# Optimization experiments

Hardware: AMD Instinct MI355X
Metric: run time of the kernel (lower is better)

The kernel has to match this reference:

```python
import jax, jax.numpy as jnp
import numpy as np

N, E, IN, HID, OUT = 100000, 1600000, 128, 128, 64


def setup_inputs() -> dict:
    key = jax.random.key(0)
    k1, k2, k3, k4 = jax.random.split(key, 4)
    x = jax.random.normal(k1, (N, IN), dtype=jnp.float32)
    edge_index = jax.random.randint(k2, (2, E), 0, N, dtype=jnp.int64)
    W1 = jax.random.normal(k3, (IN, HID), dtype=jnp.float32) * (1.0 / np.sqrt(IN))
    b1 = jnp.zeros((HID,), dtype=jnp.float32)
    W2 = jax.random.normal(k4, (HID, OUT), dtype=jnp.float32) * (1.0 / np.sqrt(HID))
    b2 = jnp.zeros((OUT,), dtype=jnp.float32)
    return {"x": x, "edge_index": edge_index, "W1": W1, "b1": b1, "W2": W2, "b2": b2}


def _gcn_conv(x, src, dst, norm, W, b):
    # linear transform first (PyG order when reducing feature dim), then SpMM
    h = x @ W                                   # [N, F_out]
    msg = h[src] * norm[:, None]                # [E+N, F_out] gathered messages
    out = jax.ops.segment_sum(msg, dst, num_segments=x.shape[0])
    return out + b


def _norm_coeffs(edge_index, num_nodes, dtype):
    # add self-loops and compute symmetric normalization deg^-1/2[src]*deg^-1/2[dst]
    loop = jnp.arange(num_nodes, dtype=edge_index.dtype)
    src = jnp.concatenate([edge_index[0], loop])
    dst = jnp.concatenate([edge_index[1], loop])
    deg = jax.ops.segment_sum(jnp.ones_like(dst, dtype=dtype), dst, num_segments=num_nodes)
    dinv = jnp.where(deg > 0, jax.lax.rsqrt(jnp.maximum(deg, 1.0)), 0.0)
    norm = dinv[src] * dinv[dst]
    return src, dst, norm


def reference(x, edge_index, W1, b1, W2, b2):
    # eval-mode forward: dropout is identity
    src, dst, norm = _norm_coeffs(edge_index, x.shape[0], x.dtype)
    h = jax.nn.relu(_gcn_conv(x, src, dst, norm, W1, b1))
    out = _gcn_conv(h, src, dst, norm, W2, b2)
    return out
```

## Files before the change

kernel.cpp:

```cpp
#include <hip/hip_runtime.h>
#include <hip/hip_bf16.h>

#define DEVINL __device__ __forceinline__

typedef __attribute__((ext_vector_type(8))) short bf16x8;
typedef __attribute__((ext_vector_type(4))) float f32x4;

union U8 {
    bf16x8 v;
    uint4 u;
};

DEVINL int clampidx(int v, int n) { return ((unsigned)v < (unsigned)n) ? v : 0; }
DEVINL float bflo(unsigned int u) { return __uint_as_float(u << 16); }
DEVINL float bfhi(unsigned int u) { return __uint_as_float(u & 0xffff0000u); }
DEVINL unsigned int f2bf(float f) {
    unsigned int u = __float_as_uint(f);
    u += 0x7fffu + ((u >> 16) & 1u);
    return u >> 16;
}

DEVINL void split8(const float4 v0, const float4 v1, uint4& hi, uint4& lo) {
    const float xv[8] = {v0.x, v0.y, v0.z, v0.w, v1.x, v1.y, v1.z, v1.w};
    unsigned h[8], l[8];
#pragma unroll
    for (int j = 0; j < 8; ++j) {
        h[j] = f2bf(xv[j]);
        const float r = xv[j] - bflo(h[j]);
        l[j] = f2bf(r);
    }
    hi = make_uint4(h[0] | (h[1] << 16), h[2] | (h[3] << 16),
                    h[4] | (h[5] << 16), h[6] | (h[7] << 16));
    lo = make_uint4(l[0] | (l[1] << 16), l[2] | (l[3] << 16),
                    l[4] | (l[5] << 16), l[6] | (l[7] << 16));
}

__global__ __launch_bounds__(256) void k_count_wprep(
    const int* __restrict__ ei, int* __restrict__ bktCnt, int E, int n,
    const float* __restrict__ W1, const float* __restrict__ W2,
    unsigned short* __restrict__ WT1h, unsigned short* __restrict__ WT1l,
    unsigned short* __restrict__ WT2h, unsigned short* __restrict__ WT2l) {
    __shared__ int hist[1024];
    const int gi = blockIdx.x * 256 + threadIdx.x;
    if (gi < 16384) {
        const int nn = gi & 127, k = gi >> 7;
        const float v = W1[k * 128 + nn];
        const unsigned h = f2bf(v);
        const float r = v - bflo(h);
        WT1h[nn * 128 + k] = (unsigned short)h;
        WT1l[nn * 128 + k] = (unsigned short)f2bf(r);
    }
    if (gi < 8192) {
        const int nn = gi & 63, k = gi >> 6;
        const float v = W2[k * 64 + nn];
        const unsigned h = f2bf(v);
        const float r = v - bflo(h);
        WT2h[nn * 128 + k] = (unsigned short)h;
        WT2l[nn * 128 + k] = (unsigned short)f2bf(r);
    }
    for (int i = threadIdx.x; i < 1024; i += 256) hist[i] = 0;
    __syncthreads();
    const int base = blockIdx.x * 4096;
#pragma unroll
    for (int j = 0; j < 16; ++j) {
        int i = base + j * 256 + threadIdx.x;
        if (i < E) atomicAdd(&hist[clampidx(ei[(size_t)E + i], n) >> 7], 1);
    }
    __syncthreads();
    for (int b = threadIdx.x; b < 1024; b += 256) {
        int c = hist[b];
        if (c) atomicAdd(&bktCnt[b], c);
    }
}

__global__ __launch_bounds__(256) void k_bktscan(const int* __restrict__ bktCnt,
                                                 int* __restrict__ bktBase,
                                                 int* __restrict__ bktCur, int NB) {
    __shared__ int sh[256];
    int carry = 0;
    for (int c0 = 0; c0 < NB; c0 += 256) {
        const int i = c0 + threadIdx.x;
        const int v = (i < NB) ? bktCnt[i] : 0;
        sh[threadIdx.x] = v;
        __syncthreads();
        for (int off = 1; off < 256; off <<= 1) {
            int t = (threadIdx.x >= off) ? sh[threadIdx.x - off] : 0;
            __syncthreads();
            sh[threadIdx.x] += t;
            __syncthreads();
        }
        if (i < NB) {
            const int excl = carry + sh[threadIdx.x] - v;
            bktBase[i] = excl;
            bktCur[i] = excl;
        }
        const int tot = sh[255];
        __syncthreads();
        carry += tot;
    }
    if (threadIdx.x == 0) bktBase[NB] = carry;
}

__global__ __launch_bounds__(256) void k_bktscatter(const int* __restrict__ ei,
                                                    int* __restrict__ bktCur,
                                                    unsigned int* __restrict__ packed,
                                                    int E, int n) {
    __shared__ unsigned int sPack[4096];
    __shared__ unsigned short sBkt[4096];
    __shared__ int sHist[1024], sStart[1024], sLoc[1024];
    for (int i = threadIdx.x; i < 1024; i += 256) {
        sHist[i] = 0;
        sLoc[i] = 0;
    }
    __syncthreads();
    const int base = blockIdx.x * 4096;
#pragma unroll
    for (int j = 0; j < 16; ++j) {
        const int k = j * 256 + threadIdx.x;
        const int i = base + k;
        if (i < E) {
            const int s = clampidx(ei[i], n);
            const int d = clampidx(ei[(size_t)E + i], n);
            const int b = d >> 7;
            sPack[k] = ((unsigned)(d & 127) << 25) | (unsigned)s;
            sBkt[k] = (unsigned short)b;
            atomicAdd(&sHist[b], 1);
        }
    }
    __syncthreads();
    for (int b = threadIdx.x; b < 1024; b += 256) {
        const int c = sHist[b];
        sStart[b] = c ? atomicAdd(&bktCur[b], c) : 0;
    }
    __syncthreads();
#pragma unroll
    for (int j = 0; j < 16; ++j) {
        const int k = j * 256 + threadIdx.x;
        const int i = base + k;
        if (i < E) {
            const int b = sBkt[k];
            const int pos = sStart[b] + atomicAdd(&sLoc[b], 1);
            packed[pos] = sPack[k];
        }
    }
}

__global__ __launch_bounds__(256) void k_bktfill(const unsigned int* __restrict__ packed,
                                                 const int* __restrict__ bktBase,
                                                 int* __restrict__ p, float* __restrict__ dinv,
                                                 int* __restrict__ srcs, int n) {
    constexpr int CAP = 8192;
    __shared__ unsigned int sPack[CAP];
    __shared__ int sSrc[CAP];
    __shared__ int deg[128], incl[128], cur[128];
    const int bkt = blockIdx.x;
    const int e0 = bktBase[bkt], e1 = bktBase[bkt + 1];
    const int cnt = e1 - e0;
    const int tid = threadIdx.x;
    if (tid < 128) deg[tid] = 0;
    __syncthreads();
    for (int i = tid; i < cnt; i += 256) {
        const unsigned int u = packed[e0 + i];
        if (i < CAP) sPack[i] = u;
        atomicAdd(&deg[u >> 25], 1);
    }
    __syncthreads();
    if (tid < 128) incl[tid] = deg[tid];
    __syncthreads();
    for (int off = 1; off < 128; off <<= 1) {
        const int v = (tid < 128 && tid >= off) ? incl[tid - off] : 0;
        __syncthreads();
        if (tid < 128) incl[tid] += v;
        __syncthreads();
    }
    const int node0 = bkt << 7;
    if (tid < 128) {
        cur[tid] = incl[tid] - deg[tid];
        const int node = node0 + tid;
        if (node < n) {
            p[node] = e0 + incl[tid];
            dinv[node] = rsqrtf((float)deg[tid] + 1.0f);
        }
    }
    __syncthreads();
    for (int i = tid; i < cnt; i += 256) {
        const unsigned int u = (i < CAP) ? sPack[i] : packed[e0 + i];
        const int dl = (int)(u >> 25);
        const int s = (int)(u & 0x1FFFFFFu);
        const int pos = atomicAdd(&cur[dl], 1);
        if (pos < CAP) sSrc[pos] = s;
        else srcs[e0 + pos] = s;
    }
    __syncthreads();
    const int lim = cnt < CAP ? cnt : CAP;
    for (int i = tid; i < lim; i += 256) srcs[e0 + i] = sSrc[i];
}

__global__ __launch_bounds__(256) void k_gemm1(const float* __restrict__ x,
                                               const unsigned short* __restrict__ WTh,
                                               const unsigned short* __restrict__ WTl,
                                               unsigned short* __restrict__ Y16, int n) {
    const int lane = threadIdx.x & 63;
    const int row16 = lane & 15;
    const int kg = lane >> 4;
    const int rowbase = blockIdx.x * 128 + (threadIdx.x >> 6) * 32;

    U8 ahi[2][4], alo[2][4];
#pragma unroll
    for (int g = 0; g < 2; ++g) {
        const int grow = rowbase + g * 16 + row16;
        if (grow < n) {
            const float* xp = x + (size_t)grow * 128 + kg * 8;
#pragma unroll
            for (int k0 = 0; k0 < 4; ++k0) {
                const float4 v0 = *(const float4*)(xp + k0 * 32);
                const float4 v1 = *(const float4*)(xp + k0 * 32 + 4);
                split8(v0, v1, ahi[g][k0].u, alo[g][k0].u);
            }
        } else {
#pragma unroll
            for (int k0 = 0; k0 < 4; ++k0) {
                ahi[g][k0].u = make_uint4(0, 0, 0, 0);
                alo[g][k0].u = make_uint4(0, 0, 0, 0);
            }
        }
    }

    f32x4 acc[2][8];
#pragma unroll
    for (int g = 0; g < 2; ++g)
#pragma unroll
        for (int nt = 0; nt < 8; ++nt) acc[g][nt] = (f32x4){0.f, 0.f, 0.f, 0.f};

#pragma unroll
    for (int nt = 0; nt < 8; ++nt) {
        const unsigned short* bp = WTh + (size_t)(nt * 16 + row16) * 128 + kg * 8;
        const unsigned short* bq = WTl + (size_t)(nt * 16 + row16) * 128 + kg * 8;
#pragma unroll
        for (int k0 = 0; k0 < 4; ++k0) {
            U8 bh, bl;
            bh.u = *(const uint4*)(bp + k0 * 32);
            bl.u = *(const uint4*)(bq + k0 * 32);
            acc[0][nt] = __builtin_amdgcn_mfma_f32_16x16x32_bf16(ahi[0][k0].v, bh.v, acc[0][nt], 0, 0, 0);
            acc[0][nt] = __builtin_amdgcn_mfma_f32_16x16x32_bf16(alo[0][k0].v, bh.v, acc[0][nt], 0, 0, 0);
            acc[0][nt] = __builtin_amdgcn_mfma_f32_16x16x32_bf16(ahi[0][k0].v, bl.v, acc[0][nt], 0, 0, 0);
            acc[1][nt] = __builtin_amdgcn_mfma_f32_16x16x32_bf16(ahi[1][k0].v, bh.v, acc[1][nt], 0, 0, 0);
            acc[1][nt] = __builtin_amdgcn_mfma_f32_16x16x32_bf16(alo[1][k0].v, bh.v, acc[1][nt], 0, 0, 0);
            acc[1][nt] = __builtin_amdgcn_mfma_f32_16x16x32_bf16(ahi[1][k0].v, bl.v, acc[1][nt], 0, 0, 0);
        }
    }

    const int m4 = (lane >> 4) * 4;
#pragma unroll
    for (int g = 0; g < 2; ++g)
#pragma unroll
        for (int nt = 0; nt < 8; ++nt) {
#pragma unroll
            for (int r = 0; r < 4; ++r) {
                const int orow = rowbase + g * 16 + m4 + r;
                if (orow < n)
                    Y16[(size_t)orow * 128 + nt * 16 + row16] =
                        (unsigned short)f2bf(acc[g][nt][r]);
            }
        }
}

__global__ __launch_bounds__(256) void k_gemm2_mfma(const unsigned short* __restrict__ H16,
                                                    const unsigned short* __restrict__ WTh,
                                                    const unsigned short* __restrict__ WTl,
                                                    unsigned short* __restrict__ Y16, int n) {
    const int lane = threadIdx.x & 63;
    const int row16 = lane & 15;
    const int kg = lane >> 4;
    const int rowbase = blockIdx.x * 64 + (threadIdx.x >> 6) * 16;
    const int grow = rowbase + row16;

    U8 a[4];
    if (grow < n) {
        const unsigned short* ap = H16 + (size_t)grow * 128 + kg * 8;
#pragma unroll
        for (int k0 = 0; k0 < 4; ++k0) a[k0].u = *(const uint4*)(ap + k0 * 32);
    } else {
#pragma unroll
        for (int k0 = 0; k0 < 4; ++k0) a[k0].u = make_uint4(0, 0, 0, 0);
    }

    f32x4 acc[4];
#pragma unroll
    for (int nt = 0; nt < 4; ++nt) acc[nt] = (f32x4){0.f, 0.f, 0.f, 0.f};

#pragma unroll
    for (int nt = 0; nt < 4; ++nt) {
        const unsigned short* bp = WTh + (size_t)(nt * 16 + row16) * 128 + kg * 8;
        const unsigned short* bq = WTl + (size_t)(nt * 16 + row16) * 128 + kg * 8;
#pragma unroll
        for (int k0 = 0; k0 < 4; ++k0) {
            U8 bh, bl;
            bh.u = *(const uint4*)(bp + k0 * 32);
            bl.u = *(const uint4*)(bq + k0 * 32);
            acc[nt] = __builtin_amdgcn_mfma_f32_16x16x32_bf16(a[k0].v, bh.v, acc[nt], 0, 0, 0);
            acc[nt] = __builtin_amdgcn_mfma_f32_16x16x32_bf16(a[k0].v, bl.v, acc[nt], 0, 0, 0);
        }
    }

    const int m4 = (lane >> 4) * 4;
#pragma unroll
    for (int nt = 0; nt < 4; ++nt) {
#pragma unroll
        for (int r = 0; r < 4; ++r) {
            const int orow = rowbase + m4 + r;
            if (orow < n)
                Y16[(size_t)orow * 64 + nt * 16 + row16] = (unsigned short)f2bf(acc[nt][r]);
        }
    }
}

__global__ __launch_bounds__(256) void k_gather128(const unsigned int* __restrict__ XW,
                                                   const int* __restrict__ p,
                                                   const int* __restrict__ srcs,
                                                   const float* __restrict__ dinv,
                                                   const float* __restrict__ b1,
                                                   unsigned int* __restrict__ H1b, int n) {
    const int node = __builtin_amdgcn_readfirstlane(blockIdx.x * 4 + (threadIdx.x >> 6));
    if (node >= n) return;
    const int t = threadIdx.x & 63;
    const int start = (node == 0) ? 0 : p[node - 1];
    const int end = p[node];
    const float din = dinv[node];
    const unsigned int us = XW[(size_t)node * 64 + t];
    float a0 = bflo(us) * din, a1 = bfhi(us) * din;

    int c = start;
    for (; c + 16 <= end; c += 16) {
        int s[16];
#pragma unroll
        for (int k = 0; k < 16; ++k) s[k] = __builtin_amdgcn_readfirstlane(srcs[c + k]);
        float w[16];
        unsigned int u[16];
#pragma unroll
        for (int k = 0; k < 16; ++k) {
            w[k] = dinv[s[k]];
            u[k] = XW[((unsigned)s[k] << 6) + t];
        }
#pragma unroll
        for (int k = 0; k < 16; ++k) {
            a0 = fmaf(bflo(u[k]), w[k], a0);
            a1 = fmaf(bfhi(u[k]), w[k], a1);
        }
    }
    for (; c + 4 <= end; c += 4) {
        int s[4];
#pragma unroll
        for (int k = 0; k < 4; ++k) s[k] = __builtin_amdgcn_readfirstlane(srcs[c + k]);
        float w[4];
        unsigned int u[4];
#pragma unroll
        for (int k = 0; k < 4; ++k) {
            w[k] = dinv[s[k]];
            u[k] = XW[((unsigned)s[k] << 6) + t];
        }
#pragma unroll
        for (int k = 0; k < 4; ++k) {
            a0 = fmaf(bflo(u[k]), w[k], a0);
            a1 = fmaf(bfhi(u[k]), w[k], a1);
        }
    }
    for (; c < end; ++c) {
        const int s = __builtin_amdgcn_readfirstlane(srcs[c]);
        const float w = dinv[s];
        const unsigned int u = XW[((unsigned)s << 6) + t];
        a0 = fmaf(bflo(u), w, a0);
        a1 = fmaf(bfhi(u), w, a1);
    }
    const float r0 = fmaxf(fmaf(a0, din, b1[2 * t]), 0.0f);
    const float r1 = fmaxf(fmaf(a1, din, b1[2 * t + 1]), 0.0f);
    H1b[(size_t)node * 64 + t] = f2bf(r0) | (f2bf(r1) << 16);
}

__global__ __launch_bounds__(256) void k_gather64(const unsigned short* __restrict__ h2,
                                                  const int* __restrict__ p,
                                                  const int* __restrict__ srcs,
                                                  const float* __restrict__ dinv,
                                                  const float* __restrict__ b2,
                                                  float* __restrict__ out, int n) {
    const int node = __builtin_amdgcn_readfirstlane(blockIdx.x * 4 + (threadIdx.x >> 6));
    if (node >= n) return;
    const int t = threadIdx.x & 63;
    const int start = (node == 0) ? 0 : p[node - 1];
    const int end = p[node];
    const float din = dinv[node];
    float acc = bflo(h2[(size_t)node * 64 + t]) * din;

    int c = start;
    for (; c + 16 <= end; c += 16) {
        int s[16];
#pragma unroll
        for (int k = 0; k < 16; ++k) s[k] = __builtin_amdgcn_readfirstlane(srcs[c + k]);
        float w[16], v[16];
#pragma unroll
        for (int k = 0; k < 16; ++k) {
            w[k] = dinv[s[k]];
            v[k] = bflo(h2[((unsigned)s[k] << 6) + t]);
        }
#pragma unroll
        for (int k = 0; k < 16; ++k) acc = fmaf(v[k], w[k], acc);
    }
    for (; c + 4 <= end; c += 4) {
        int s[4];
#pragma unroll
        for (int k = 0; k < 4; ++k) s[k] = __builtin_amdgcn_readfirstlane(srcs[c + k]);
        float w[4], v[4];
#pragma unroll
        for (int k = 0; k < 4; ++k) {
            w[k] = dinv[s[k]];
            v[k] = bflo(h2[((unsigned)s[k] << 6) + t]);
        }
#pragma unroll
        for (int k = 0; k < 4; ++k) acc = fmaf(v[k], w[k], acc);
    }
    for (; c < end; ++c) {
        const int s = __builtin_amdgcn_readfirstlane(srcs[c]);
        const float w = dinv[s];
        acc = fmaf(bflo(h2[((unsigned)s << 6) + t]), w, acc);
    }
    out[(size_t)node * 64 + t] = fmaf(acc, din, b2[t]);
}

extern "C" void kernel_launch(void* const* d_in, const int* in_sizes, int n_in,
                              void* d_out, int out_size, void* d_ws, size_t ws_size,
                              hipStream_t stream) {
    const float* x  = (const float*)d_in[0];
    const int* ei   = (const int*)d_in[1];
    const float* W1 = (const float*)d_in[2];
    const float* b1 = (const float*)d_in[3];
    const float* W2 = (const float*)d_in[4];
    const float* b2 = (const float*)d_in[5];

    const int n = in_sizes[0] / 128;
    const int E = in_sizes[1] / 2;
    const int NB = (n + 127) >> 7;

    auto al = [](size_t b) { return (b + 255) & ~(size_t)255; };
    const size_t off_p    = 0;
    const size_t off_dinv = off_p + al((size_t)n * 4);
    const size_t off_srcs = off_dinv + al((size_t)n * 4);
    const size_t off_XW   = off_srcs + al((size_t)E * 4);
    const size_t off_H1b  = off_XW + al((size_t)n * 64 * 4);
    const size_t off_w1h  = off_H1b + al((size_t)n * 64 * 4);
    const size_t off_w1l  = off_w1h + al(128 * 128 * 2);
    const size_t off_w2h  = off_w1l + al(128 * 128 * 2);
    const size_t off_w2l  = off_w2h + al(64 * 128 * 2);
    const size_t need     = off_w2l + (size_t)64 * 128 * 2;
    const size_t off_pk   = off_H1b;
    const size_t off_bc   = off_pk + al((size_t)E * 4);
    const size_t off_bb   = off_bc + al(1024 * 4);
    const size_t off_bu   = off_bb + al(1025 * 4);
    const size_t csr_end  = off_bu + (size_t)1024 * 4;

    if (ws_size < need || NB > 1024 || csr_end > off_w1h) {
        hipMemsetAsync(d_out, 0, (size_t)out_size * 4, stream);
        return;
    }

    int*            p    = (int*)((char*)d_ws + off_p);
    float*          dinv = (float*)((char*)d_ws + off_dinv);
    int*            srcs = (int*)((char*)d_ws + off_srcs);
    unsigned int*   XW   = (unsigned int*)((char*)d_ws + off_XW);
    unsigned int*   H1b  = (unsigned int*)((char*)d_ws + off_H1b);
    unsigned int*   pk   = (unsigned int*)((char*)d_ws + off_pk);
    int*            bCnt = (int*)((char*)d_ws + off_bc);
    int*            bBase= (int*)((char*)d_ws + off_bb);
    int*            bCur = (int*)((char*)d_ws + off_bu);
    unsigned short* WT1h = (unsigned short*)((char*)d_ws + off_w1h);
    unsigned short* WT1l = (unsigned short*)((char*)d_ws + off_w1l);
    unsigned short* WT2h = (unsigned short*)((char*)d_ws + off_w2h);
    unsigned short* WT2l = (unsigned short*)((char*)d_ws + off_w2l);
    float*          out  = (float*)d_out;

    const int gEdge = (E + 4095) / 4096;
    const int gM1   = (n + 127) / 128;
    const int gM2   = (n + 63) / 64;
    const int gG    = (n + 3) / 4;

    hipMemsetAsync(bCnt, 0, 1024 * 4, stream);

    k_count_wprep<<<gEdge, 256, 0, stream>>>(ei, bCnt, E, n, W1, W2, WT1h, WT1l, WT2h, WT2l);

    k_gemm1<<<gM1, 256, 0, stream>>>(x, WT1h, WT1l, (unsigned short*)XW, n);

    k_bktscan<<<1, 256, 0, stream>>>(bCnt, bBase, bCur, NB);
    k_bktscatter<<<gEdge, 256, 0, stream>>>(ei, bCur, pk, E, n);
    k_bktfill<<<NB, 256, 0, stream>>>(pk, bBase, p, dinv, srcs, n);

    k_gather128<<<gG, 256, 0, stream>>>(XW, p, srcs, dinv, b1, H1b, n);

    k_gemm2_mfma<<<gM2, 256, 0, stream>>>((const unsigned short*)H1b, WT2h, WT2l,
                                          (unsigned short*)XW, n);

    k_gather64<<<gG, 256, 0, stream>>>((const unsigned short*)XW, p, srcs, dinv, b2, out, n);
}
```

Before: 343.9 us.

## Replace atomic bucket reservation with per-block histogram prefix scan

The count kernel now writes a per-block bucket histogram instead of atomically adding into global counters. A new column-wise scan kernel computes each block's deterministic offset within every bucket plus the bucket totals. The scatter kernel then starts from precomputed offsets, dropping its local histogram pass and its global atomics. This removes the memset and the contention on bucket counters, at the cost of an extra kernel launch and a strided read/write of a gEdge×1024 offset table.

Result: no change. 346.9 us (+0.9%).

```diff
diff --git a/kernel.cpp b/kernel.cpp
--- a/kernel.cpp
+++ b/kernel.cpp
@@ -36,7 +36,7 @@
 }
 
 __global__ __launch_bounds__(256) void k_count_wprep(
-    const int* __restrict__ ei, int* __restrict__ bktCnt, int E, int n,
+    const int* __restrict__ ei, int* __restrict__ blkHist, int E, int n,
     const float* __restrict__ W1, const float* __restrict__ W2,
     unsigned short* __restrict__ WT1h, unsigned short* __restrict__ WT1l,
     unsigned short* __restrict__ WT2h, unsigned short* __restrict__ WT2l) {
@@ -67,20 +67,43 @@
         if (i < E) atomicAdd(&hist[clampidx(ei[(size_t)E + i], n) >> 7], 1);
     }
     __syncthreads();
-    for (int b = threadIdx.x; b < 1024; b += 256) {
-        int c = hist[b];
-        if (c) atomicAdd(&bktCnt[b], c);
-    }
-}
-
-__global__ __launch_bounds__(256) void k_bktscan(const int* __restrict__ bktCnt,
-                                                 int* __restrict__ bktBase,
-                                                 int* __restrict__ bktCur, int NB) {
+    int* row = blkHist + (size_t)blockIdx.x * 1024;
+    for (int b = threadIdx.x; b < 1024; b += 256) row[b] = hist[b];
+}
+
+__global__ __launch_bounds__(256) void k_blkscan(const int* __restrict__ blkHist,
+                                                 int* __restrict__ blkOff,
+                                                 int* __restrict__ bktTot, int nBlk) {
+    __shared__ int sh[1024];
+    const int b = blockIdx.x;
+    const int tid = threadIdx.x;
+    for (int i = tid; i < 1024; i += 256)
+        sh[i] = (i < nBlk) ? blkHist[(size_t)i * 1024 + b] : 0;
+    __syncthreads();
+    for (int off = 1; off < 1024; off <<= 1) {
+        int t[4];
+#pragma unroll
+        for (int j = 0; j < 4; ++j) {
+            const int i = tid + j * 256;
+            t[j] = (i >= off) ? sh[i - off] : 0;
+        }
+        __syncthreads();
+#pragma unroll
+        for (int j = 0; j < 4; ++j) sh[tid + j * 256] += t[j];
+        __syncthreads();
+    }
+    for (int i = tid; i < nBlk; i += 256)
+        blkOff[(size_t)i * 1024 + b] = (i == 0) ? 0 : sh[i - 1];
+    if (tid == 0) bktTot[b] = sh[nBlk - 1];
+}
+
+__global__ __launch_bounds__(256) void k_bktscan(const int* __restrict__ bktTot,
+                                                 int* __restrict__ bktBase, int NB) {
     __shared__ int sh[256];
     int carry = 0;
     for (int c0 = 0; c0 < NB; c0 += 256) {
         const int i = c0 + threadIdx.x;
-        const int v = (i < NB) ? bktCnt[i] : 0;
+        const int v = (i < NB) ? bktTot[i] : 0;
         sh[threadIdx.x] = v;
         __syncthreads();
         for (int off = 1; off < 256; off <<= 1) {
@@ -89,11 +112,7 @@
             sh[threadIdx.x] += t;
             __syncthreads();
         }
-        if (i < NB) {
-            const int excl = carry + sh[threadIdx.x] - v;
-            bktBase[i] = excl;
-            bktCur[i] = excl;
-        }
+        if (i < NB) bktBase[i] = carry + sh[threadIdx.x] - v;
         const int tot = sh[255];
         __syncthreads();
         carry += tot;
@@ -102,15 +121,17 @@
 }
 
 __global__ __launch_bounds__(256) void k_bktscatter(const int* __restrict__ ei,
-                                                    int* __restrict__ bktCur,
+                                                    const int* __restrict__ bktBase,
+                                                    const int* __restrict__ blkOff,
                                                     unsigned int* __restrict__ packed,
                                                     int E, int n) {
     __shared__ unsigned int sPack[4096];
     __shared__ unsigned short sBkt[4096];
-    __shared__ int sHist[1024], sStart[1024], sLoc[1024];
-    for (int i = threadIdx.x; i < 1024; i += 256) {
-        sHist[i] = 0;
-        sLoc[i] = 0;
+    __shared__ int sStart[1024], sLoc[1024];
+    const int* offrow = blkOff + (size_t)blockIdx.x * 1024;
+    for (int b = threadIdx.x; b < 1024; b += 256) {
+        sStart[b] = bktBase[b] + offrow[b];
+        sLoc[b] = 0;
     }
     __syncthreads();
     const int base = blockIdx.x * 4096;
@@ -124,13 +145,7 @@
             const int b = d >> 7;
             sPack[k] = ((unsigned)(d & 127) << 25) | (unsigned)s;
             sBkt[k] = (unsigned short)b;
-            atomicAdd(&sHist[b], 1);
-        }
-    }
-    __syncthreads();
-    for (int b = threadIdx.x; b < 1024; b += 256) {
-        const int c = sHist[b];
-        sStart[b] = c ? atomicAdd(&bktCur[b], c) : 0;
+        }
     }
     __syncthreads();
 #pragma unroll
@@ -439,6 +454,7 @@
     const int n = in_sizes[0] / 128;
     const int E = in_sizes[1] / 2;
     const int NB = (n + 127) >> 7;
+    const int gEdge = (E + 4095) / 4096;
 
     auto al = [](size_t b) { return (b + 255) & ~(size_t)255; };
     const size_t off_p    = 0;
@@ -452,12 +468,13 @@
     const size_t off_w2l  = off_w2h + al(64 * 128 * 2);
     const size_t need     = off_w2l + (size_t)64 * 128 * 2;
     const size_t off_pk   = off_H1b;
-    const size_t off_bc   = off_pk + al((size_t)E * 4);
-    const size_t off_bb   = off_bc + al(1024 * 4);
-    const size_t off_bu   = off_bb + al(1025 * 4);
-    const size_t csr_end  = off_bu + (size_t)1024 * 4;
-
-    if (ws_size < need || NB > 1024 || csr_end > off_w1h) {
+    const size_t off_bh   = off_pk + al((size_t)E * 4);
+    const size_t off_bo   = off_bh + al((size_t)gEdge * 1024 * 4);
+    const size_t off_bt   = off_bo + al((size_t)gEdge * 1024 * 4);
+    const size_t off_bb   = off_bt + al(1024 * 4);
+    const size_t csr_end  = off_bb + (size_t)1025 * 4;
+
+    if (ws_size < need || NB > 1024 || gEdge > 1024 || csr_end > off_w1h) {
         hipMemsetAsync(d_out, 0, (size_t)out_size * 4, stream);
         return;
     }
@@ -468,28 +485,28 @@
     unsigned int*   XW   = (unsigned int*)((char*)d_ws + off_XW);
     unsigned int*   H1b  = (unsigned int*)((char*)d_ws + off_H1b);
     unsigned int*   pk   = (unsigned int*)((char*)d_ws + off_pk);
-    int*            bCnt = (int*)((char*)d_ws + off_bc);
+    int*            blkH = (int*)((char*)d_ws + off_bh);
+    int*            blkO = (int*)((char*)d_ws + off_bo);
+    int*            bTot = (int*)((char*)d_ws + off_bt);
     int*            bBase= (int*)((char*)d_ws + off_bb);
-    int*            bCur = (int*)((char*)d_ws + off_bu);
     unsigned short* WT1h = (unsigned short*)((char*)d_ws + off_w1h);
     unsigned short* WT1l = (unsigned short*)((char*)d_ws + off_w1l);
     unsigned short* WT2h = (unsigned short*)((char*)d_ws + off_w2h);
     unsigned short* WT2l = (unsigned short*)((char*)d_ws + off_w2l);
     float*          out  = (float*)d_out;
 
-    const int gEdge = (E + 4095) / 4096;
-    const int gM1   = (n + 127) / 128;
-    const int gM2   = (n + 63) / 64;
-    const int gG    = (n + 3) / 4;
-
-    hipMemsetAsync(bCnt, 0, 1024 * 4, stream);
-
-    k_count_wprep<<<gEdge, 256, 0, stream>>>(ei, bCnt, E, n, W1, W2, WT1h, WT1l, WT2h, WT2l);
+    const int gM1 = (n + 127) / 128;
+    const int gM2 = (n + 63) / 64;
+    const int gG  = (n + 3) / 4;
+
+    k_count_wprep<<<gEdge, 256, 0, stream>>>(ei, blkH, E, n, W1, W2, WT1h, WT1l, WT2h, WT2l);
 
     k_gemm1<<<gM1, 256, 0, stream>>>(x, WT1h, WT1l, (unsigned short*)XW, n);
 
-    k_bktscan<<<1, 256, 0, stream>>>(bCnt, bBase, bCur, NB);
-    k_bktscatter<<<gEdge, 256, 0, stream>>>(ei, bCur, pk, E, n);
+    k_blkscan<<<1024, 256, 0, stream>>>(blkH, blkO, bTot, gEdge);
+    k_bktscan<<<1, 256, 0, stream>>>(bTot, bBase, NB);
+
+    k_bktscatter<<<gEdge, 256, 0, stream>>>(ei, bBase, blkO, pk, E, n);
     k_bktfill<<<NB, 256, 0, stream>>>(pk, bBase, p, dinv, srcs, n);
 
     k_gather128<<<gG, 256, 0, stream>>>(XW, p, srcs, dinv, b1, H1b, n);
```

## Split layer-1 gather into feature halves pinned per XCD half for cache locality

Applied to the files above, without the earlier changes.

The 128-wide layer-1 SpMM gather is split into two 64-feature halves. Each block reads a hardware register (s_getreg) to learn which half of the chip it runs on, then takes work tickets from a per-half atomic counter, falling back to the other half's counter once its own is exhausted. The goal is for each XCD group to touch only half of the XW feature table, so the random-gather working set fits better in each die's L2. Each block also processes 16 node groups in a loop. In exchange, every lane now does 2-byte loads instead of 4-byte ones, issues twice as many gathers per edge, and the kernel depends on a register-field interpretation plus an extra memset for the tickets.

Measured after the change: 413.6 us. 1.2x slower.

```diff
diff --git a/kernel.cpp b/kernel.cpp
--- a/kernel.cpp
+++ b/kernel.cpp
@@ -14,6 +14,7 @@
 DEVINL int clampidx(int v, int n) { return ((unsigned)v < (unsigned)n) ? v : 0; }
 DEVINL float bflo(unsigned int u) { return __uint_as_float(u << 16); }
 DEVINL float bfhi(unsigned int u) { return __uint_as_float(u & 0xffff0000u); }
+DEVINL float bf16f(unsigned int u16) { return __uint_as_float(u16 << 16); }
 DEVINL unsigned int f2bf(float f) {
     unsigned int u = __float_as_uint(f);
     u += 0x7fffu + ((u >> 16) & 1u);
@@ -315,66 +316,79 @@
     }
 }
 
-__global__ __launch_bounds__(256) void k_gather128(const unsigned int* __restrict__ XW,
-                                                   const int* __restrict__ p,
-                                                   const int* __restrict__ srcs,
-                                                   const float* __restrict__ dinv,
-                                                   const float* __restrict__ b1,
-                                                   unsigned int* __restrict__ H1b, int n) {
-    const int node = __builtin_amdgcn_readfirstlane(blockIdx.x * 4 + (threadIdx.x >> 6));
-    if (node >= n) return;
+__global__ __launch_bounds__(256) void k_gather128(
+    const unsigned short* __restrict__ XW, const int* __restrict__ p,
+    const int* __restrict__ srcs, const float* __restrict__ dinv,
+    const float* __restrict__ b1, unsigned short* __restrict__ H1b, int n,
+    int* __restrict__ tickets, int nGroups, int nch, int G) {
+    __shared__ int sT, sH;
+    if (threadIdx.x == 0) {
+        int h = __builtin_amdgcn_s_getreg((3 << 11) | 20) & 1;
+        int t = atomicAdd(&tickets[h], 1);
+        if (t >= nch) {
+            h ^= 1;
+            t = atomicAdd(&tickets[h], 1);
+            if (t >= nch) t = -1;
+        }
+        sT = t;
+        sH = h;
+    }
+    __syncthreads();
+    const int tkt = sT;
+    const int half = sH;
+    if (tkt < 0) return;
     const int t = threadIdx.x & 63;
-    const int start = (node == 0) ? 0 : p[node - 1];
-    const int end = p[node];
-    const float din = dinv[node];
-    const unsigned int us = XW[(size_t)node * 64 + t];
-    float a0 = bflo(us) * din, a1 = bfhi(us) * din;
-
-    int c = start;
-    for (; c + 16 <= end; c += 16) {
-        int s[16];
-#pragma unroll
-        for (int k = 0; k < 16; ++k) s[k] = __builtin_amdgcn_readfirstlane(srcs[c + k]);
-        float w[16];
-        unsigned int u[16];
-#pragma unroll
-        for (int k = 0; k < 16; ++k) {
-            w[k] = dinv[s[k]];
-            u[k] = XW[((unsigned)s[k] << 6) + t];
-        }
-#pragma unroll
-        for (int k = 0; k < 16; ++k) {
-            a0 = fmaf(bflo(u[k]), w[k], a0);
-            a1 = fmaf(bfhi(u[k]), w[k], a1);
-        }
-    }
-    for (; c + 4 <= end; c += 4) {
-        int s[4];
-#pragma unroll
-        for (int k = 0; k < 4; ++k) s[k] = __builtin_amdgcn_readfirstlane(srcs[c + k]);
-        float w[4];
-        unsigned int u[4];
-#pragma unroll
-        for (int k = 0; k < 4; ++k) {
-            w[k] = dinv[s[k]];
-            u[k] = XW[((unsigned)s[k] << 6) + t];
-        }
-#pragma unroll
-        for (int k = 0; k < 4; ++k) {
-            a0 = fmaf(bflo(u[k]), w[k], a0);
-            a1 = fmaf(bfhi(u[k]), w[k], a1);
-        }
-    }
-    for (; c < end; ++c) {
-        const int s = __builtin_amdgcn_readfirstlane(srcs[c]);
-        const float w = dinv[s];
-        const unsigned int u = XW[((unsigned)s << 6) + t];
-        a0 = fmaf(bflo(u), w, a0);
-        a1 = fmaf(bfhi(u), w, a1);
-    }
-    const float r0 = fmaxf(fmaf(a0, din, b1[2 * t]), 0.0f);
-    const float r1 = fmaxf(fmaf(a1, din, b1[2 * t + 1]), 0.0f);
-    H1b[(size_t)node * 64 + t] = f2bf(r0) | (f2bf(r1) << 16);
+    const int wv = threadIdx.x >> 6;
+    const int j = half * 64 + t;
+    const float bj = b1[j];
+
+    for (int it = 0; it < G; ++it) {
+        const int grp = tkt * G + it;
+        if (grp >= nGroups) break;
+        const int node = __builtin_amdgcn_readfirstlane(grp * 4 + wv);
+        if (node >= n) continue;
+        const int start = (node == 0) ? 0 : p[node - 1];
+        const int end = p[node];
+        const float din = dinv[node];
+        float a = bf16f(XW[(size_t)node * 128 + j]) * din;
+
+        int c = start;
+        for (; c + 16 <= end; c += 16) {
+            int s[16];
+#pragma unroll
+            for (int k = 0; k < 16; ++k) s[k] = __builtin_amdgcn_readfirstlane(srcs[c + k]);
+            float w[16];
+            unsigned int u[16];
+#pragma unroll
+            for (int k = 0; k < 16; ++k) {
+                w[k] = dinv[s[k]];
+                u[k] = XW[(size_t)s[k] * 128 + j];
+            }
+#pragma unroll
+            for (int k = 0; k < 16; ++k) a = fmaf(bf16f(u[k]), w[k], a);
+        }
+        for (; c + 4 <= end; c += 4) {
+            int s[4];
+#pragma unroll
+            for (int k = 0; k < 4; ++k) s[k] = __builtin_amdgcn_readfirstlane(srcs[c + k]);
+            float w[4];
+            unsigned int u[4];
+#pragma unroll
+            for (int k = 0; k < 4; ++k) {
+                w[k] = dinv[s[k]];
+                u[k] = XW[(size_t)s[k] * 128 + j];
+            }
+#pragma unroll
+            for (int k = 0; k < 4; ++k) a = fmaf(bf16f(u[k]), w[k], a);
+        }
+        for (; c < end; ++c) {
+            const int s = __builtin_amdgcn_readfirstlane(srcs[c]);
+            const float w = dinv[s];
+            a = fmaf(bf16f(XW[(size_t)s * 128 + j]), w, a);
+        }
+        const float r = fmaxf(fmaf(a, din, bj), 0.0f);
+        H1b[(size_t)node * 128 + j] = (unsigned short)f2bf(r);
+    }
 }
 
 __global__ __launch_bounds__(256) void k_gather64(const unsigned short* __restrict__ h2,
@@ -450,7 +464,8 @@
     const size_t off_w1l  = off_w1h + al(128 * 128 * 2);
     const size_t off_w2h  = off_w1l + al(128 * 128 * 2);
     const size_t off_w2l  = off_w2h + al(64 * 128 * 2);
-    const size_t need     = off_w2l + (size_t)64 * 128 * 2;
+    const size_t off_tk   = off_w2l + al(64 * 128 * 2);
+    const size_t need     = off_tk + 256;
     const size_t off_pk   = off_H1b;
     const size_t off_bc   = off_pk + al((size_t)E * 4);
     const size_t off_bb   = off_bc + al(1024 * 4);
@@ -475,6 +490,7 @@
     unsigned short* WT1l = (unsigned short*)((char*)d_ws + off_w1l);
     unsigned short* WT2h = (unsigned short*)((char*)d_ws + off_w2h);
     unsigned short* WT2l = (unsigned short*)((char*)d_ws + off_w2l);
+    int*            tk   = (int*)((char*)d_ws + off_tk);
     float*          out  = (float*)d_out;
 
     const int gEdge = (E + 4095) / 4096;
@@ -482,7 +498,12 @@
     const int gM2   = (n + 63) / 64;
     const int gG    = (n + 3) / 4;
 
+    const int nGroups = gG;
+    const int G       = 16;
+    const int nch     = (nGroups + G - 1) / G;
+
     hipMemsetAsync(bCnt, 0, 1024 * 4, stream);
+    hipMemsetAsync(tk, 0, 256, stream);
 
     k_count_wprep<<<gEdge, 256, 0, stream>>>(ei, bCnt, E, n, W1, W2, WT1h, WT1l, WT2h, WT2l);
 
@@ -492,7 +513,8 @@
     k_bktscatter<<<gEdge, 256, 0, stream>>>(ei, bCur, pk, E, n);
     k_bktfill<<<NB, 256, 0, stream>>>(pk, bBase, p, dinv, srcs, n);
 
-    k_gather128<<<gG, 256, 0, stream>>>(XW, p, srcs, dinv, b1, H1b, n);
+    k_gather128<<<2 * nch, 256, 0, stream>>>((const unsigned short*)XW, p, srcs, dinv, b1,
+                                             (unsigned short*)H1b, n, tk, nGroups, nch, G);
 
     k_gemm2_mfma<<<gM2, 256, 0, stream>>>((const unsigned short*)H1b, WT2h, WT2l,
                                           (unsigned short*)XW, n);
```

## Replace bucketed CSR build with per-node atomic count, scan and scatter

Applied to the files above, without the earlier changes.

The two-level CSR construction (1024 coarse buckets, a shared-memory histogram, a bucket scatter, then an in-bucket fill) is replaced by a direct scheme. Each edge does a global atomicAdd on its destination's degree. A two-kernel scan then builds the row pointers, the per-node cursors and dinv, and a final kernel scatters each source with a global atomicAdd on its node's cursor. This removes the intermediate packed buffer and the shared-memory bucket passes. In exchange it relies on many global atomics to scattered addresses and makes the neighbour order within a row nondeterministic.

Measured after the change: 491.9 us. 1.43x slower.

```diff
diff --git a/kernel.cpp b/kernel.cpp
--- a/kernel.cpp
+++ b/kernel.cpp
@@ -36,11 +36,10 @@
 }
 
 __global__ __launch_bounds__(256) void k_count_wprep(
-    const int* __restrict__ ei, int* __restrict__ bktCnt, int E, int n,
+    const int* __restrict__ ei, int* __restrict__ deg, int E, int n,
     const float* __restrict__ W1, const float* __restrict__ W2,
     unsigned short* __restrict__ WT1h, unsigned short* __restrict__ WT1l,
     unsigned short* __restrict__ WT2h, unsigned short* __restrict__ WT2l) {
-    __shared__ int hist[1024];
     const int gi = blockIdx.x * 256 + threadIdx.x;
     if (gi < 16384) {
         const int nn = gi & 127, k = gi >> 7;
@@ -58,142 +57,79 @@
         WT2h[nn * 128 + k] = (unsigned short)h;
         WT2l[nn * 128 + k] = (unsigned short)f2bf(r);
     }
-    for (int i = threadIdx.x; i < 1024; i += 256) hist[i] = 0;
+    if (gi < E) atomicAdd(&deg[clampidx(ei[(size_t)E + gi], n)], 1);
+}
+
+__global__ __launch_bounds__(256) void k_scan1(const int* __restrict__ deg,
+                                               int* __restrict__ p,
+                                               int* __restrict__ blkSum, int n) {
+    __shared__ int sh[256];
+    const int tid = threadIdx.x;
+    const int i0 = blockIdx.x * 1024 + tid * 4;
+    int4 d = make_int4(0, 0, 0, 0);
+    if (i0 + 3 < n) d = *(const int4*)&deg[i0];
+    else {
+        if (i0 < n) d.x = deg[i0];
+        if (i0 + 1 < n) d.y = deg[i0 + 1];
+        if (i0 + 2 < n) d.z = deg[i0 + 2];
+    }
+    const int s1 = d.x, s2 = s1 + d.y, s3 = s2 + d.z, s4 = s3 + d.w;
+    sh[tid] = s4;
     __syncthreads();
-    const int base = blockIdx.x * 4096;
-#pragma unroll
-    for (int j = 0; j < 16; ++j) {
-        int i = base + j * 256 + threadIdx.x;
-        if (i < E) atomicAdd(&hist[clampidx(ei[(size_t)E + i], n) >> 7], 1);
-    }
+    for (int off = 1; off < 256; off <<= 1) {
+        int t = (tid >= off) ? sh[tid - off] : 0;
+        __syncthreads();
+        sh[tid] += t;
+        __syncthreads();
+    }
+    const int excl = sh[tid] - s4;
+    if (i0 < n) p[i0] = excl + s1;
+    if (i0 + 1 < n) p[i0 + 1] = excl + s2;
+    if (i0 + 2 < n) p[i0 + 2] = excl + s3;
+    if (i0 + 3 < n) p[i0 + 3] = excl + s4;
+    if (tid == 255) blkSum[blockIdx.x] = sh[255];
+}
+
+__global__ __launch_bounds__(256) void k_finalize(int* __restrict__ p,
+                                                  const int* __restrict__ blkSum,
+                                                  const int* __restrict__ deg,
+                                                  int* __restrict__ cur,
+                                                  float* __restrict__ dinv, int n) {
+    __shared__ int red[256];
+    const int tid = threadIdx.x;
+    int partial = 0;
+    for (int j = tid; j < (int)blockIdx.x; j += 256) partial += blkSum[j];
+    red[tid] = partial;
     __syncthreads();
-    for (int b = threadIdx.x; b < 1024; b += 256) {
-        int c = hist[b];
-        if (c) atomicAdd(&bktCnt[b], c);
-    }
-}
-
-__global__ __launch_bounds__(256) void k_bktscan(const int* __restrict__ bktCnt,
-                                                 int* __restrict__ bktBase,
-                                                 int* __restrict__ bktCur, int NB) {
-    __shared__ int sh[256];
-    int carry = 0;
-    for (int c0 = 0; c0 < NB; c0 += 256) {
-        const int i = c0 + threadIdx.x;
-        const int v = (i < NB) ? bktCnt[i] : 0;
-        sh[threadIdx.x] = v;
+    for (int off = 128; off > 0; off >>= 1) {
+        if (tid < off) red[tid] += red[tid + off];
         __syncthreads();
-        for (int off = 1; off < 256; off <<= 1) {
-            int t = (threadIdx.x >= off) ? sh[threadIdx.x - off] : 0;
-            __syncthreads();
-            sh[threadIdx.x] += t;
-            __syncthreads();
-        }
-        if (i < NB) {
-            const int excl = carry + sh[threadIdx.x] - v;
-            bktBase[i] = excl;
-            bktCur[i] = excl;
-        }
-        const int tot = sh[255];
-        __syncthreads();
-        carry += tot;
-    }
-    if (threadIdx.x == 0) bktBase[NB] = carry;
-}
-
-__global__ __launch_bounds__(256) void k_bktscatter(const int* __restrict__ ei,
-                                                    int* __restrict__ bktCur,
-                                                    unsigned int* __restrict__ packed,
-                                                    int E, int n) {
-    __shared__ unsigned int sPack[4096];
-    __shared__ unsigned short sBkt[4096];
-    __shared__ int sHist[1024], sStart[1024], sLoc[1024];
-    for (int i = threadIdx.x; i < 1024; i += 256) {
-        sHist[i] = 0;
-        sLoc[i] = 0;
-    }
-    __syncthreads();
-    const int base = blockIdx.x * 4096;
-#pragma unroll
-    for (int j = 0; j < 16; ++j) {
-        const int k = j * 256 + threadIdx.x;
-        const int i = base + k;
-        if (i < E) {
-            const int s = clampidx(ei[i], n);
-            const int d = clampidx(ei[(size_t)E + i], n);
-            const int b = d >> 7;
-            sPack[k] = ((unsigned)(d & 127) << 25) | (unsigned)s;
-            sBkt[k] = (unsigned short)b;
-            atomicAdd(&sHist[b], 1);
-        }
-    }
-    __syncthreads();
-    for (int b = threadIdx.x; b < 1024; b += 256) {
-        const int c = sHist[b];
-        sStart[b] = c ? atomicAdd(&bktCur[b], c) : 0;
-    }
-    __syncthreads();
-#pragma unroll
-    for (int j = 0; j < 16; ++j) {
-        const int k = j * 256 + threadIdx.x;
-        const int i = base + k;
-        if (i < E) {
-            const int b = sBkt[k];
-            const int pos = sStart[b] + atomicAdd(&sLoc[b], 1);
-            packed[pos] = sPack[k];
-        }
-    }
-}
-
-__global__ __launch_bounds__(256) void k_bktfill(const unsigned int* __restrict__ packed,
-                                                 const int* __restrict__ bktBase,
-                                                 int* __restrict__ p, float* __restrict__ dinv,
-                                                 int* __restrict__ srcs, int n) {
-    constexpr int CAP = 8192;
-    __shared__ unsigned int sPack[CAP];
-    __shared__ int sSrc[CAP];
-    __shared__ int deg[128], incl[128], cur[128];
-    const int bkt = blockIdx.x;
-    const int e0 = bktBase[bkt], e1 = bktBase[bkt + 1];
-    const int cnt = e1 - e0;
-    const int tid = threadIdx.x;
-    if (tid < 128) deg[tid] = 0;
-    __syncthreads();
-    for (int i = tid; i < cnt; i += 256) {
-        const unsigned int u = packed[e0 + i];
-        if (i < CAP) sPack[i] = u;
-        atomicAdd(&deg[u >> 25], 1);
-    }
-    __syncthreads();
-    if (tid < 128) incl[tid] = deg[tid];
-    __syncthreads();
-    for (int off = 1; off < 128; off <<= 1) {
-        const int v = (tid < 128 && tid >= off) ? incl[tid - off] : 0;
-        __syncthreads();
-        if (tid < 128) incl[tid] += v;
-        __syncthreads();
-    }
-    const int node0 = bkt << 7;
-    if (tid < 128) {
-        cur[tid] = incl[tid] - deg[tid];
-        const int node = node0 + tid;
-        if (node < n) {
-            p[node] = e0 + incl[tid];
-            dinv[node] = rsqrtf((float)deg[tid] + 1.0f);
-        }
-    }
-    __syncthreads();
-    for (int i = tid; i < cnt; i += 256) {
-        const unsigned int u = (i < CAP) ? sPack[i] : packed[e0 + i];
-        const int dl = (int)(u >> 25);
-        const int s = (int)(u & 0x1FFFFFFu);
-        const int pos = atomicAdd(&cur[dl], 1);
-        if (pos < CAP) sSrc[pos] = s;
-        else srcs[e0 + pos] = s;
-    }
-    __syncthreads();
-    const int lim = cnt < CAP ? cnt : CAP;
-    for (int i = tid; i < lim; i += 256) srcs[e0 + i] = sSrc[i];
+    }
+    const int off0 = red[0];
+    const int i0 = blockIdx.x * 1024 + tid * 4;
+#pragma unroll
+    for (int j = 0; j < 4; ++j) {
+        const int i = i0 + j;
+        if (i < n) {
+            const int pi = p[i] + off0;
+            const int dg = deg[i];
+            p[i] = pi;
+            cur[i] = pi - dg;
+            dinv[i] = rsqrtf((float)dg + 1.0f);
+        }
+    }
+}
+
+__global__ __launch_bounds__(256) void k_scatter(const int* __restrict__ ei,
+                                                 int* __restrict__ cur,
+                                                 int* __restrict__ srcs, int E, int n) {
+    const int i = blockIdx.x * 256 + threadIdx.x;
+    if (i < E) {
+        const int s = clampidx(ei[i], n);
+        const int d = clampidx(ei[(size_t)E + i], n);
+        const int pos = atomicAdd(&cur[d], 1);
+        srcs[pos] = s;
+    }
 }
 
 __global__ __launch_bounds__(256) void k_gemm1(const float* __restrict__ x,
@@ -438,7 +374,6 @@
 
     const int n = in_sizes[0] / 128;
     const int E = in_sizes[1] / 2;
-    const int NB = (n + 127) >> 7;
 
     auto al = [](size_t b) { return (b + 255) & ~(size_t)255; };
     const size_t off_p    = 0;
@@ -451,13 +386,13 @@
     const size_t off_w2h  = off_w1l + al(128 * 128 * 2);
     const size_t off_w2l  = off_w2h + al(64 * 128 * 2);
     const size_t need     = off_w2l + (size_t)64 * 128 * 2;
-    const size_t off_pk   = off_H1b;
-    const size_t off_bc   = off_pk + al((size_t)E * 4);
-    const size_t off_bb   = off_bc + al(1024 * 4);
-    const size_t off_bu   = off_bb + al(1025 * 4);
-    const size_t csr_end  = off_bu + (size_t)1024 * 4;
-
-    if (ws_size < need || NB > 1024 || csr_end > off_w1h) {
+    const int nBlkScan    = (n + 1023) / 1024;
+    const size_t off_dg   = off_H1b;
+    const size_t off_cu   = off_dg + al((size_t)n * 4);
+    const size_t off_bs   = off_cu + al((size_t)n * 4);
+    const size_t csr_end  = off_bs + al((size_t)nBlkScan * 4);
+
+    if (ws_size < need || csr_end > off_w1h) {
         hipMemsetAsync(d_out, 0, (size_t)out_size * 4, stream);
         return;
     }
@@ -467,30 +402,29 @@
     int*            srcs = (int*)((char*)d_ws + off_srcs);
     unsigned int*   XW   = (unsigned int*)((char*)d_ws + off_XW);
     unsigned int*   H1b  = (unsigned int*)((char*)d_ws + off_H1b);
-    unsigned int*   pk   = (unsigned int*)((char*)d_ws + off_pk);
-    int*            bCnt = (int*)((char*)d_ws + off_bc);
-    int*            bBase= (int*)((char*)d_ws + off_bb);
-    int*            bCur = (int*)((char*)d_ws + off_bu);
+    int*            deg  = (int*)((char*)d_ws + off_dg);
+    int*            cur  = (int*)((char*)d_ws + off_cu);
+    int*            bSum = (int*)((char*)d_ws + off_bs);
     unsigned short* WT1h = (unsigned short*)((char*)d_ws + off_w1h);
     unsigned short* WT1l = (unsigned short*)((char*)d_ws + off_w1l);
     unsigned short* WT2h = (unsigned short*)((char*)d_ws + off_w2h);
     unsigned short* WT2l = (unsigned short*)((char*)d_ws + off_w2l);
     float*          out  = (float*)d_out;
 
-    const int gEdge = (E + 4095) / 4096;
-    const int gM1   = (n + 127) / 128;
-    const int gM2   = (n + 63) / 64;
-    const int gG    = (n + 3) / 4;
-
-    hipMemsetAsync(bCnt, 0, 1024 * 4, stream);
-
-    k_count_wprep<<<gEdge, 256, 0, stream>>>(ei, bCnt, E, n, W1, W2, WT1h, WT1l, WT2h, WT2l);
+    const int gE  = (E + 255) / 256;
+    const int gM1 = (n + 127) / 128;
+    const int gM2 = (n + 63) / 64;
+    const int gG  = (n + 3) / 4;
+
+    hipMemsetAsync(deg, 0, (size_t)n * 4, stream);
+
+    k_count_wprep<<<gE, 256, 0, stream>>>(ei, deg, E, n, W1, W2, WT1h, WT1l, WT2h, WT2l);
 
     k_gemm1<<<gM1, 256, 0, stream>>>(x, WT1h, WT1l, (unsigned short*)XW, n);
 
-    k_bktscan<<<1, 256, 0, stream>>>(bCnt, bBase, bCur, NB);
-    k_bktscatter<<<gEdge, 256, 0, stream>>>(ei, bCur, pk, E, n);
-    k_bktfill<<<NB, 256, 0, stream>>>(pk, bBase, p, dinv, srcs, n);
+    k_scan1<<<nBlkScan, 256, 0, stream>>>(deg, p, bSum, n);
+    k_finalize<<<nBlkScan, 256, 0, stream>>>(p, bSum, deg, cur, dinv, n);
+    k_scatter<<<gE, 256, 0, stream>>>(ei, cur, srcs, E, n);
 
     k_gather128<<<gG, 256, 0, stream>>>(XW, p, srcs, dinv, b1, H1b, n);
 
```
